# Performance work log

Measured on AMD Instinct MI355X. Metric: run time of the kernel, lower is better.

The kernel has to match this reference:

```python
import jax, jax.numpy as jnp
import numpy as np

H, W = 192, 640  # image feature-map size (x_rgb[0].shape[2:])


def _pts2img(coor, feat):
    """coor: [N,2] normalized (u,v) in [0,1]; feat: [N,C] -> [C,H,W].
    Mirrors pts2img: swap to (v,u), scale by (H,W), truncate to int,
    last-write-wins scatter into (H+1,W+1,C), crop the overflow row/col."""
    coor = jnp.clip(coor, 0.0, 1.0)
    rc = (coor[:, ::-1] * jnp.array([H, W], coor.dtype)).astype(jnp.int32)  # [N,2] (row,col)
    grid = jnp.zeros((H + 1, W + 1, feat.shape[1]), feat.dtype)
    grid = grid.at[rc[:, 0], rc[:, 1]].set(feat)
    return grid[:H, :W].transpose(2, 0, 1)  # [C,H,W]


def _conv1x1(x, Wm, b):
    # x: [B,C,H,W], Wm: [O,C]
    return jnp.einsum('bchw,oc->bohw', x, Wm) + b[None, :, None, None]


def _conv3x3(x, Wk, b):
    y = jax.lax.conv_general_dilated(x, Wk, window_strides=(1, 1),
                                     padding=((1, 1), (1, 1)),
                                     dimension_numbers=('NCHW', 'OIHW', 'NCHW'))
    return y + b[None, :, None, None]


def setup_inputs() -> dict:
    key = jax.random.key(0)
    ks = jax.random.split(key, 16)
    B, C_IMG = 2, 64
    N0, C0 = 40000, 32
    N1, C1 = 20000, 64
    CL = C1 + 3  # 67
    s = 0.05
    return {
        'x_rgb0': jax.random.normal(ks[0], (B, C_IMG, H, W), jnp.float32),
        'feat0': jax.random.normal(ks[1], (B, N0, C0), jnp.float32),
        'coor0': jax.random.uniform(ks[2], (B, N0, 2), jnp.float32),
        'vox0': jax.random.normal(ks[3], (B, N0, 3), jnp.float32),
        'feat1': jax.random.normal(ks[4], (B, N1, C1), jnp.float32),
        'coor1': jax.random.uniform(ks[5], (B, N1, 2), jnp.float32),
        'vox1': jax.random.normal(ks[6], (B, N1, 3), jnp.float32),
        'W_red0': s * jax.random.normal(ks[7], (CL, C0 + 3), jnp.float32),
        'b_red0': s * jax.random.normal(ks[8], (CL,), jnp.float32),
        'W_red2': s * jax.random.normal(ks[9], (CL, CL), jnp.float32),
        'b_red2': s * jax.random.normal(ks[10], (CL,), jnp.float32),
        'W_red3': s * jax.random.normal(ks[11], (1, C_IMG), jnp.float32),
        'b_red3': s * jax.random.normal(ks[12], (1,), jnp.float32),
        'W_sp': s * jax.random.normal(ks[13], (1, CL, 3, 3), jnp.float32),
        'b_sp': s * jax.random.normal(ks[14], (1,), jnp.float32),
    }


def reference(x_rgb0, feat0, coor0, vox0, feat1, coor1, vox1,
              W_red0, b_red0, W_red2, b_red2, W_red3, b_red3, W_sp, b_sp):
    scatter = jax.vmap(_pts2img)  # over batch
    # level features = cat(sparse features, 3D voxel coords)
    pts_img0 = scatter(coor0, jnp.concatenate([feat0, vox0], axis=-1))  # [B,35,H,W]
    pts_img1 = scatter(coor1, jnp.concatenate([feat1, vox1], axis=-1))  # [B,67,H,W]
    # voxel_idx = [0,1]: 1x1 reduce on level 0, residual add of level 1
    enhanced = _conv1x1(pts_img0, W_red0, b_red0) + pts_img1
    enhanced = _conv1x1(enhanced, W_red2, b_red2)
    gated = _conv1x1(x_rgb0, W_red3, b_red3)  # [B,1,H,W], broadcasts over 67 ch
    fused = gated + enhanced
    att = jax.nn.sigmoid(_conv3x3(fused, W_sp, b_sp))  # [B,1,H,W]
    return x_rgb0 * att
```

## Files before the change

kernel.cpp:

```cpp
#include <hip/hip_runtime.h>

namespace {
constexpr int kH = 192, kW = 640, kHW = kH * kW;
constexpr int kW4g = kW / 4;
constexpr int kHW4 = kHW / 4;
constexpr int kB = 2, kC = 64;
constexpr int kN0 = 40000, kC0 = 32;
constexpr int kN1 = 20000, kC1 = 64;
constexpr int kCL = 67;
constexpr int kBHW = kB * kHW;
constexpr int kPH = kH + 2, kPW = kW + 8;
constexpr int kPW4 = kPW / 4;
constexpr int kPlane = kPH * kPW;
constexpr int kYPF = 18 * kPlane;
constexpr int kWin4 = 2 * kBHW / 4;
constexpr int kBord = 162 + 162 + 192 * 2;
constexpr int kBordTot = 18 * kBord;
constexpr int kScatB = 469;
constexpr int kGateB0 = 470;
constexpr int kGateB = kB * kHW4 / 64;
constexpr int kChunks = kB * kHW4 / 256;

typedef float vf4 __attribute__((ext_vector_type(4)));

__global__ __launch_bounds__(256) void kinit(float* __restrict__ yp,
                                             int4* __restrict__ win4) {
  int i = blockIdx.x * 256 + threadIdx.x;
  if (i < kBordTot) {
    int plane = i / kBord, r = i - plane * kBord;
    float4* base = (float4*)(yp + (size_t)plane * kPlane);
    int f4;
    if (r < 162) {
      f4 = r;
    } else if (r < 324) {
      f4 = 193 * kPW4 + (r - 162);
    } else {
      int rr = r - 324;
      int row = 1 + (rr >> 1);
      f4 = row * kPW4 + ((rr & 1) ? (kPW4 - 1) : 0);
    }
    base[f4] = make_float4(0.f, 0.f, 0.f, 0.f);
  } else {
    int j = i - kBordTot;
    if (j < kWin4) win4[j] = make_int4(-1, -1, -1, -1);
  }
}

__global__ __launch_bounds__(256) void k2(
    const float* __restrict__ coor0, const float* __restrict__ coor1,
    int* __restrict__ win0, int* __restrict__ win1,
    const float* __restrict__ W0, const float* __restrict__ b0,
    const float* __restrict__ W2, const float* __restrict__ b2,
    const float* __restrict__ Wsp, float* __restrict__ M0,
    float* __restrict__ A1g, float* __restrict__ sb, float* __restrict__ wsum,
    const float* __restrict__ x_rgb, const float* __restrict__ W3,
    float* __restrict__ g) {
  __shared__ float W2s[kCL * kCL];
  __shared__ float W0s[kCL * 35];
  __shared__ float Wsps[kCL * 9];
  __shared__ float A1s[9 * kCL];
  __shared__ float bps[kCL];
  const int bid = blockIdx.x;
  const int t = threadIdx.x;
  if (bid >= kGateB0) {
    __shared__ float4 part[4][64];
    const int gg = t & 63, q = t >> 6;
    const int gran = (bid - kGateB0) * 64 + gg;
    const int b = gran / kHW4;
    const int p4 = gran - b * kHW4;
    const float4* xr = (const float4*)(x_rgb + (size_t)b * kC * kHW) + p4;
    float4 acc = make_float4(0.f, 0.f, 0.f, 0.f);
#pragma unroll
    for (int cc = 0; cc < 16; ++cc) {
      const int c = q * 16 + cc;
      float wv = W3[c];
      float4 x4 = xr[(size_t)c * kHW4];
      acc.x += wv * x4.x;
      acc.y += wv * x4.y;
      acc.z += wv * x4.z;
      acc.w += wv * x4.w;
    }
    part[q][gg] = acc;
    __syncthreads();
    if (t < 64) {
      float4 p0 = part[0][t], p1 = part[1][t], p2 = part[2][t],
             p3 = part[3][t];
      float4 s;
      s.x = p0.x + p1.x + p2.x + p3.x;
      s.y = p0.y + p1.y + p2.y + p3.y;
      s.z = p0.z + p1.z + p2.z + p3.z;
      s.w = p0.w + p1.w + p2.w + p3.w;
      ((float4*)g)[(bid - kGateB0) * 64 + t] = s;
    }
    return;
  }
  if (bid < kScatB) {
    int idx = bid * 256 + t;
    const float* coor;
    int* win;
    int N;
    if (idx < kB * kN0) {
      coor = coor0; win = win0; N = kN0;
    } else {
      idx -= kB * kN0;
      if (idx >= kB * kN1) return;
      coor = coor1; win = win1; N = kN1;
    }
    int b = idx / N;
    float u = coor[(size_t)idx * 2 + 0];
    float v = coor[(size_t)idx * 2 + 1];
    u = fminf(fmaxf(u, 0.f), 1.f);
    v = fminf(fmaxf(v, 0.f), 1.f);
    int r = (int)(v * (float)kH);
    int c = (int)(u * (float)kW);
    if (r < kH && c < kW) {
      int n = idx - b * N;
      atomicMax(&win[b * kHW + r * kW + c], n);
    }
    return;
  }
  for (int i = t; i < kCL * kCL; i += 256) W2s[i] = W2[i];
  for (int i = t; i < kCL * 35; i += 256) W0s[i] = W0[i];
  for (int i = t; i < kCL * 9; i += 256) Wsps[i] = Wsp[i];
  __syncthreads();
  if (t < kCL) {
    float s = b2[t];
    for (int j = 0; j < kCL; ++j) s += W2s[t * kCL + j] * b0[j];
    bps[t] = s;
  }
  for (int idx = t; idx < 9 * kCL; idx += 256) {
    int k = idx / kCL, j = idx - k * kCL;
    float s = 0.f;
    for (int c = 0; c < kCL; ++c) s += Wsps[c * 9 + k] * W2s[c * kCL + j];
    A1s[idx] = s;
    A1g[idx] = s;
  }
  __syncthreads();
  for (int idx = t; idx < 9 * 35; idx += 256) {
    int k = idx / 35, i = idx - k * 35;
    float s = 0.f;
    for (int j = 0; j < kCL; ++j) s += A1s[k * kCL + j] * W0s[j * 35 + i];
    M0[idx] = s;
  }
  if (t < 9) {
    float s = 0.f;
    for (int c = 0; c < kCL; ++c) s += Wsps[c * 9 + t] * bps[c];
    sb[t] = s;
  } else if (t >= 16 && t < 25) {
    int k = t - 16;
    float s = 0.f;
    for (int c = 0; c < kCL; ++c) s += Wsps[c * 9 + k];
    wsum[k] = s;
  }
}

__global__ __launch_bounds__(256) void kgy(
    const float* __restrict__ g, const int* __restrict__ win0,
    const int* __restrict__ win1, const float* __restrict__ feat0,
    const float* __restrict__ vox0, const float* __restrict__ feat1,
    const float* __restrict__ vox1, const float* __restrict__ M0,
    const float* __restrict__ A1, const float* __restrict__ sb,
    const float* __restrict__ wsum, const float* __restrict__ b3,
    float* __restrict__ yp) {
  const int blk = blockIdx.x;
  const int tg = blk % 3;
  const int pix = (blk / 3) * 256 + threadIdx.x;
  const int b = pix / kHW;
  const int pp = pix - b * kHW;
  const int h = pp / kW;
  const int w = pp - h * kW;
  const float gv = b3[0] + g[pix];
  float y[3];
#pragma unroll
  for (int kk = 0; kk < 3; ++kk)
    y[kk] = wsum[3 * tg + kk] * gv + sb[3 * tg + kk];

  const int w0 = win0[pix];
  if (w0 >= 0) {
    const float4* f0 = (const float4*)(feat0 + ((size_t)b * kN0 + w0) * kC0);
#pragma unroll
    for (int i4 = 0; i4 < 8; ++i4) {
      float4 v = f0[i4];
#pragma unroll
      for (int kk = 0; kk < 3; ++kk) {
        const float* m = M0 + (3 * tg + kk) * 35 + i4 * 4;
        y[kk] += m[0] * v.x + m[1] * v.y + m[2] * v.z + m[3] * v.w;
      }
    }
    const float* v0 = vox0 + ((size_t)b * kN0 + w0) * 3;
#pragma unroll
    for (int i = 0; i < 3; ++i) {
      float v = v0[i];
#pragma unroll
      for (int kk = 0; kk < 3; ++kk)
        y[kk] += M0[(3 * tg + kk) * 35 + kC0 + i] * v;
    }
  }
  const int w1 = win1[pix];
  if (w1 >= 0) {
    const float4* f1 = (const float4*)(feat1 + ((size_t)b * kN1 + w1) * kC1);
#pragma unroll
    for (int i4 = 0; i4 < 16; ++i4) {
      float4 v = f1[i4];
#pragma unroll
      for (int kk = 0; kk < 3; ++kk) {
        const float* m = A1 + (3 * tg + kk) * kCL + i4 * 4;
        y[kk] += m[0] * v.x + m[1] * v.y + m[2] * v.z + m[3] * v.w;
      }
    }
    const float* v1 = vox1 + ((size_t)b * kN1 + w1) * 3;
#pragma unroll
    for (int i = 0; i < 3; ++i) {
      float v = v1[i];
#pragma unroll
      for (int kk = 0; kk < 3; ++kk)
        y[kk] += A1[(3 * tg + kk) * kCL + kC1 + i] * v;
    }
  }
#pragma unroll
  for (int kk = 0; kk < 3; ++kk) {
    yp[((size_t)((3 * tg + kk) * kB + b) * kPH + (h + 1)) * kPW + 4 + w] =
        y[kk];
  }
}

__global__ __launch_bounds__(256) void kpass2(const float* __restrict__ x_rgb,
                                              const float* __restrict__ yp,
                                              const float* __restrict__ bsp,
                                              float* __restrict__ out) {
  const int bid = blockIdx.x;
  const int q = bid / kChunks;
  const int chunk = bid - q * kChunks;
  const int gran = chunk * 256 + threadIdx.x;
  const int b = gran / kHW4;
  const int p4 = gran - b * kHW4;
  const int h = p4 / kW4g;
  const int w4 = p4 - h * kW4g;

  const float bias = bsp[0];
  float4 lg = make_float4(bias, bias, bias, bias);
#pragma unroll
  for (int r = 0; r < 3; ++r) {
    const size_t rowoff = ((size_t)h + r) * kPW + 4 * w4;
    const float* pA = yp + (size_t)((3 * r + 0) * kB + b) * kPlane + rowoff;
    const float* pB = yp + (size_t)((3 * r + 1) * kB + b) * kPlane + rowoff;
    const float* pC = yp + (size_t)((3 * r + 2) * kB + b) * kPlane + rowoff;
    float LA = pA[3];
    float4 a4 = *(const float4*)(pA + 4);
    float4 b4 = *(const float4*)(pB + 4);
    float4 c4 = *(const float4*)(pC + 4);
    float RC = pC[8];
    lg.x += LA + b4.x + c4.y;
    lg.y += a4.x + b4.y + c4.z;
    lg.z += a4.y + b4.z + c4.w;
    lg.w += a4.z + b4.w + RC;
  }
  float4 att;
  att.x = 1.f / (1.f + __expf(-lg.x));
  att.y = 1.f / (1.f + __expf(-lg.y));
  att.z = 1.f / (1.f + __expf(-lg.z));
  att.w = 1.f / (1.f + __expf(-lg.w));

  const vf4* xr = (const vf4*)(x_rgb + (size_t)b * kC * kHW) + p4;
  vf4* op = (vf4*)(out + (size_t)b * kC * kHW) + p4;
#pragma unroll
  for (int cc = 0; cc < 32; ++cc) {
    const int c = q * 32 + cc;
    vf4 x4 = __builtin_nontemporal_load(xr + (size_t)c * kHW4);
    vf4 r4;
    r4.x = x4.x * att.x;
    r4.y = x4.y * att.y;
    r4.z = x4.z * att.z;
    r4.w = x4.w * att.w;
    __builtin_nontemporal_store(r4, op + (size_t)c * kHW4);
  }
}

}

extern "C" void kernel_launch(void* const* d_in, const int* in_sizes, int n_in,
                              void* d_out, int out_size, void* d_ws,
                              size_t ws_size, hipStream_t stream) {
  const float* x_rgb = (const float*)d_in[0];
  const float* feat0 = (const float*)d_in[1];
  const float* coor0 = (const float*)d_in[2];
  const float* vox0 = (const float*)d_in[3];
  const float* feat1 = (const float*)d_in[4];
  const float* coor1 = (const float*)d_in[5];
  const float* vox1 = (const float*)d_in[6];
  const float* W0 = (const float*)d_in[7];
  const float* b0 = (const float*)d_in[8];
  const float* W2 = (const float*)d_in[9];
  const float* b2 = (const float*)d_in[10];
  const float* W3 = (const float*)d_in[11];
  const float* b3 = (const float*)d_in[12];
  const float* Wsp = (const float*)d_in[13];
  const float* bsp = (const float*)d_in[14];
  float* out = (float*)d_out;

  float* yp = (float*)d_ws;
  float* g = yp + (size_t)kYPF;
  int* win0 = (int*)(g + (size_t)kBHW);
  int* win1 = win0 + (size_t)kBHW;
  float* M0 = (float*)(win1 + (size_t)kBHW);
  float* A1 = M0 + 9 * 35;
  float* sb = A1 + 9 * kCL;
  float* wsum = sb + 9;

  const int ninit = kBordTot + kWin4;
  kinit<<<(ninit + 255) / 256, 256, 0, stream>>>(yp, (int4*)win0);
  k2<<<kGateB0 + kGateB, 256, 0, stream>>>(coor0, coor1, win0, win1, W0, b0,
                                           W2, b2, Wsp, M0, A1, sb, wsum,
                                           x_rgb, W3, g);
  kgy<<<3 * kBHW / 256, 256, 0, stream>>>(g, win0, win1, feat0, vox0, feat1,
                                          vox1, M0, A1, sb, wsum, b3, yp);
  kpass2<<<2 * kChunks, 256, 0, stream>>>(x_rgb, yp, bsp, out);
}
```

Before: 71.67 us.

## Interleave winner maps, reorder k2 blocks gate-first, use cached loads in final pass

After: 68.80 us. 1.04x faster.

```diff
diff --git a/kernel.cpp b/kernel.cpp
--- a/kernel.cpp
+++ b/kernel.cpp
@@ -16,9 +16,10 @@
 constexpr int kWin4 = 2 * kBHW / 4;
 constexpr int kBord = 162 + 162 + 192 * 2;
 constexpr int kBordTot = 18 * kBord;
+constexpr int kGateB = kB * kHW4 / 64;
+constexpr int kScatB0 = kGateB;
 constexpr int kScatB = 469;
-constexpr int kGateB0 = 470;
-constexpr int kGateB = kB * kHW4 / 64;
+constexpr int kPrecB = kScatB0 + kScatB;
 constexpr int kChunks = kB * kHW4 / 256;
 
 typedef float vf4 __attribute__((ext_vector_type(4)));
@@ -48,7 +49,7 @@
 
 __global__ __launch_bounds__(256) void k2(
     const float* __restrict__ coor0, const float* __restrict__ coor1,
-    int* __restrict__ win0, int* __restrict__ win1,
+    int* __restrict__ win01,
     const float* __restrict__ W0, const float* __restrict__ b0,
     const float* __restrict__ W2, const float* __restrict__ b2,
     const float* __restrict__ Wsp, float* __restrict__ M0,
@@ -62,10 +63,10 @@
   __shared__ float bps[kCL];
   const int bid = blockIdx.x;
   const int t = threadIdx.x;
-  if (bid >= kGateB0) {
+  if (bid < kGateB) {
     __shared__ float4 part[4][64];
     const int gg = t & 63, q = t >> 6;
-    const int gran = (bid - kGateB0) * 64 + gg;
+    const int gran = bid * 64 + gg;
     const int b = gran / kHW4;
     const int p4 = gran - b * kHW4;
     const float4* xr = (const float4*)(x_rgb + (size_t)b * kC * kHW) + p4;
@@ -90,21 +91,20 @@
       s.y = p0.y + p1.y + p2.y + p3.y;
       s.z = p0.z + p1.z + p2.z + p3.z;
       s.w = p0.w + p1.w + p2.w + p3.w;
-      ((float4*)g)[(bid - kGateB0) * 64 + t] = s;
+      ((float4*)g)[bid * 64 + t] = s;
     }
     return;
   }
-  if (bid < kScatB) {
-    int idx = bid * 256 + t;
+  if (bid < kPrecB) {
+    int idx = (bid - kScatB0) * 256 + t;
     const float* coor;
-    int* win;
-    int N;
+    int lvl, N;
     if (idx < kB * kN0) {
-      coor = coor0; win = win0; N = kN0;
+      coor = coor0; lvl = 0; N = kN0;
     } else {
       idx -= kB * kN0;
       if (idx >= kB * kN1) return;
-      coor = coor1; win = win1; N = kN1;
+      coor = coor1; lvl = 1; N = kN1;
     }
     int b = idx / N;
     float u = coor[(size_t)idx * 2 + 0];
@@ -115,7 +115,7 @@
     int c = (int)(u * (float)kW);
     if (r < kH && c < kW) {
       int n = idx - b * N;
-      atomicMax(&win[b * kHW + r * kW + c], n);
+      atomicMax(&win01[2 * (b * kHW + r * kW + c) + lvl], n);
     }
     return;
   }
@@ -155,13 +155,12 @@
 }
 
 __global__ __launch_bounds__(256) void kgy(
-    const float* __restrict__ g, const int* __restrict__ win0,
-    const int* __restrict__ win1, const float* __restrict__ feat0,
-    const float* __restrict__ vox0, const float* __restrict__ feat1,
-    const float* __restrict__ vox1, const float* __restrict__ M0,
-    const float* __restrict__ A1, const float* __restrict__ sb,
-    const float* __restrict__ wsum, const float* __restrict__ b3,
-    float* __restrict__ yp) {
+    const float* __restrict__ g, const int2* __restrict__ win01,
+    const float* __restrict__ feat0, const float* __restrict__ vox0,
+    const float* __restrict__ feat1, const float* __restrict__ vox1,
+    const float* __restrict__ M0, const float* __restrict__ A1,
+    const float* __restrict__ sb, const float* __restrict__ wsum,
+    const float* __restrict__ b3, float* __restrict__ yp) {
   const int blk = blockIdx.x;
   const int tg = blk % 3;
   const int pix = (blk / 3) * 256 + threadIdx.x;
@@ -175,7 +174,8 @@
   for (int kk = 0; kk < 3; ++kk)
     y[kk] = wsum[3 * tg + kk] * gv + sb[3 * tg + kk];
 
-  const int w0 = win0[pix];
+  const int2 wv2 = win01[pix];
+  const int w0 = wv2.x;
   if (w0 >= 0) {
     const float4* f0 = (const float4*)(feat0 + ((size_t)b * kN0 + w0) * kC0);
 #pragma unroll
@@ -196,7 +196,7 @@
         y[kk] += M0[(3 * tg + kk) * 35 + kC0 + i] * v;
     }
   }
-  const int w1 = win1[pix];
+  const int w1 = wv2.y;
   if (w1 >= 0) {
     const float4* f1 = (const float4*)(feat1 + ((size_t)b * kN1 + w1) * kC1);
 #pragma unroll
@@ -261,12 +261,12 @@
   att.z = 1.f / (1.f + __expf(-lg.z));
   att.w = 1.f / (1.f + __expf(-lg.w));
 
-  const vf4* xr = (const vf4*)(x_rgb + (size_t)b * kC * kHW) + p4;
+  const float4* xr = (const float4*)(x_rgb + (size_t)b * kC * kHW) + p4;
   vf4* op = (vf4*)(out + (size_t)b * kC * kHW) + p4;
 #pragma unroll
   for (int cc = 0; cc < 32; ++cc) {
     const int c = q * 32 + cc;
-    vf4 x4 = __builtin_nontemporal_load(xr + (size_t)c * kHW4);
+    float4 x4 = xr[(size_t)c * kHW4];
     vf4 r4;
     r4.x = x4.x * att.x;
     r4.y = x4.y * att.y;
@@ -300,19 +300,18 @@
 
   float* yp = (float*)d_ws;
   float* g = yp + (size_t)kYPF;
-  int* win0 = (int*)(g + (size_t)kBHW);
-  int* win1 = win0 + (size_t)kBHW;
-  float* M0 = (float*)(win1 + (size_t)kBHW);
+  int* win01 = (int*)(g + (size_t)kBHW);
+  float* M0 = (float*)(win01 + (size_t)2 * kBHW);
   float* A1 = M0 + 9 * 35;
   float* sb = A1 + 9 * kCL;
   float* wsum = sb + 9;
 
   const int ninit = kBordTot + kWin4;
-  kinit<<<(ninit + 255) / 256, 256, 0, stream>>>(yp, (int4*)win0);
-  k2<<<kGateB0 + kGateB, 256, 0, stream>>>(coor0, coor1, win0, win1, W0, b0,
-                                           W2, b2, Wsp, M0, A1, sb, wsum,
-                                           x_rgb, W3, g);
-  kgy<<<3 * kBHW / 256, 256, 0, stream>>>(g, win0, win1, feat0, vox0, feat1,
-                                          vox1, M0, A1, sb, wsum, b3, yp);
+  kinit<<<(ninit + 255) / 256, 256, 0, stream>>>(yp, (int4*)win01);
+  k2<<<kPrecB + 1, 256, 0, stream>>>(coor0, coor1, win01, W0, b0, W2, b2, Wsp,
+                                     M0, A1, sb, wsum, x_rgb, W3, g);
+  kgy<<<3 * kBHW / 256, 256, 0, stream>>>(g, (const int2*)win01, feat0, vox0,
+                                          feat1, vox1, M0, A1, sb, wsum, b3,
+                                          yp);
   kpass2<<<2 * kChunks, 256, 0, stream>>>(x_rgb, yp, bsp, out);
 }
```
